# Kernel tuning notes

Hardware: AMD Instinct MI355X
Metric: run time of the kernel (lower is better)

Reference implementation:

```python
import jax, jax.numpy as jnp
import numpy as np

NUM_MODELS = 64
IN_F, HID, OUT_F = 6, 64, 3
LAYERS = 5
LN_EPS = 1e-5


def _mm_linear(x, W, B, idx):
    # W: [M, out, in], B: [M, out], x: [N, in], idx: [N]
    return jnp.einsum('nof,nf->no', W[idx], x) + B[idx]


def _mm_layernorm(x, g, b, idx):
    mu = jnp.mean(x, axis=-1, keepdims=True)
    var = jnp.mean((x - mu) ** 2, axis=-1, keepdims=True)
    xn = (x - mu) * jax.lax.rsqrt(var + LN_EPS)
    return xn * g[idx] + b[idx]


def setup_inputs() -> dict:
    key = jax.random.key(0)
    ks = jax.random.split(key, 16)
    N = 262144
    sqrt_k = float(np.sqrt(1.0 / NUM_MODELS))
    u = lambda k, shape: jax.random.uniform(k, shape, jnp.float32, -sqrt_k, sqrt_k)
    inp = {
        'x': jax.random.normal(ks[0], (N, IN_F), jnp.float32),
        'indices': jax.random.randint(ks[1], (N,), 0, NUM_MODELS),
        'W0': u(ks[2], (NUM_MODELS, HID, IN_F)), 'B0': u(ks[3], (NUM_MODELS, HID)),
        'G0': jnp.ones((NUM_MODELS, HID), jnp.float32), 'H0': jnp.zeros((NUM_MODELS, HID), jnp.float32),
        'W1': u(ks[4], (NUM_MODELS, HID, HID)), 'B1': u(ks[5], (NUM_MODELS, HID)),
        'G1': jnp.ones((NUM_MODELS, HID), jnp.float32), 'H1': jnp.zeros((NUM_MODELS, HID), jnp.float32),
        'W2': u(ks[6], (NUM_MODELS, HID, HID)), 'B2': u(ks[7], (NUM_MODELS, HID)),
        'G2': jnp.ones((NUM_MODELS, HID), jnp.float32), 'H2': jnp.zeros((NUM_MODELS, HID), jnp.float32),
        'W3': u(ks[8], (NUM_MODELS, HID, HID)), 'B3': u(ks[9], (NUM_MODELS, HID)),
        'G3': jnp.ones((NUM_MODELS, HID), jnp.float32), 'H3': jnp.zeros((NUM_MODELS, HID), jnp.float32),
        'W4': u(ks[10], (NUM_MODELS, OUT_F, HID)), 'B4': u(ks[11], (NUM_MODELS, OUT_F)),
    }
    return inp


def reference(x, indices, W0, B0, G0, H0, W1, B1, G1, H1, W2, B2, G2, H2, W3, B3, G3, H3, W4, B4):
    # forward_through_layers with use_layernorm=True, layers=5:
    Ws = [(W0, B0, G0, H0), (W1, B1, G1, H1), (W2, B2, G2, H2), (W3, B3, G3, H3)]
    h = x
    for W, B, G, Hb in Ws:
        h = _mm_linear(h, W, B, indices)
        h = _mm_layernorm(h, G, Hb, indices)
        h = jax.nn.relu(h)
    return _mm_linear(h, W4, B4, indices)  # [N, 3]
```

## Files before the change

kernel.cpp:

```cpp
#include <hip/hip_runtime.h>


#define NM    64
#define HIDD  64
#define INF   6
#define OUTF  3
#define CAP   4864
#define NBLKB 128

#define CSTRIDE   32
#define O_CURSORS 0
#define O_ORDER   2048
#define IWS_INTS  (O_ORDER + NM * CAP)

#define CONST_B   30720
#define NCONSTF   784
#define IMG_BYTES 33856

typedef _Float16 v8h __attribute__((ext_vector_type(8)));
typedef __fp16   v2hf __attribute__((ext_vector_type(2)));
typedef float    v4f __attribute__((ext_vector_type(4)));

struct BF { v8h lo, hi; };
struct PK2 { v2hf a, b; };

__device__ __host__ __forceinline__ int phi(int p) {
    int mt = p >> 4, q = (p >> 2) & 3, r = p & 3;
    return ((mt >> 1) << 5) | (q << 3) | ((mt & 1) << 2) | r;
}

__global__ __launch_bounds__(256, 4) void bucket_img_kernel(
    const int* __restrict__ idx, const float* __restrict__ x, int n,
    const float* __restrict__ W0, const float* __restrict__ W1,
    const float* __restrict__ W2, const float* __restrict__ W3,
    const float* __restrict__ W4,
    const float* __restrict__ B0, const float* __restrict__ G0, const float* __restrict__ H0,
    const float* __restrict__ B1, const float* __restrict__ G1, const float* __restrict__ H1,
    const float* __restrict__ B2, const float* __restrict__ G2, const float* __restrict__ H2,
    const float* __restrict__ B3, const float* __restrict__ G3, const float* __restrict__ H3,
    const float* __restrict__ B4,
    int* __restrict__ iws, _Float16* __restrict__ xs,
    unsigned char* __restrict__ imgbase) {
    __shared__ int lcnt[NM], lcur[NM];
    const int b = blockIdx.x, t = threadIdx.x;
    const int m = b >> 1, sub = b & 1;

    _Float16* img = (_Float16*)(imgbase + (size_t)m * IMG_BYTES);
    float* cst = (float*)(imgbase + (size_t)m * IMG_BYTES + CONST_B);
    for (int s = sub * 256 + t; s < 1920; s += 512) {
        int f = s >> 6, l = s & 63;
        int c = l & 15, q = l >> 4;
        float vals[8];
        if (f < 4) {
            const float* wr = W0 + m * 384 + phi(f * 16 + c) * 6;
#pragma unroll
            for (int j = 0; j < 8; j++) {
                int k = q * 8 + j;
                vals[j] = (k < INF) ? wr[k] : 0.0f;
            }
        } else if (f < 28) {
            int ll = (f - 4) >> 3, fb = (f - 4) & 7;
            int mt = fb >> 1, kh = fb & 1;
            const float* W = (ll == 0) ? W1 : (ll == 1) ? W2 : W3;
            const float* wr = W + m * 4096 + phi(mt * 16 + c) * 64 + kh * 32 + q * 8;
#pragma unroll
            for (int j = 0; j < 8; j++) vals[j] = wr[j];
        } else {
            int kh = f - 28;
            const float* wr = W4 + m * 192 + c * 64 + kh * 32 + q * 8;
#pragma unroll
            for (int j = 0; j < 8; j++) vals[j] = (c < OUTF) ? wr[j] : 0.0f;
        }
        v8h o;
#pragma unroll
        for (int j = 0; j < 8; j++) o[j] = (_Float16)vals[j];
        *(v8h*)(img + (size_t)s * 8) = o;
    }
    for (int e = sub * 256 + t; e < NCONSTF; e += 512) {
        const float* lsrc[12] = {B0, G0, H0, B1, G1, H1, B2, G2, H2, B3, G3, H3};
        float v = 0.0f;
        if (e < 768) {
            int l = e / 192, r = e - l * 192;
            v = lsrc[l * 3 + (r >> 6)][m * 64 + phi(r & 63)];
        } else if (e < 771) {
            v = B4[m * 3 + (e - 768)];
        }
        cst[e] = v;
    }

    if (t < NM) lcnt[t] = 0;
    __syncthreads();
    const int per = (n + NBLKB - 1) / NBLKB;
    const int beg = b * per, end = min(n, beg + per);
    for (int i = beg + t; i < end; i += 256) atomicAdd(&lcnt[idx[i]], 1);
    __syncthreads();
    if (t < NM) lcur[t] = atomicAdd(&iws[O_CURSORS + t * CSTRIDE], lcnt[t]);
    __syncthreads();
    for (int i = beg + t; i < end; i += 256) {
        int mm = idx[i];
        int r = atomicAdd(&lcur[mm], 1);
        int slot = mm * CAP + r;
        iws[O_ORDER + slot] = i;
        const float* xp = x + (size_t)i * 6;
        float2 a0 = *(const float2*)(xp);
        float2 a1 = *(const float2*)(xp + 2);
        float2 a2 = *(const float2*)(xp + 4);
        v8h o = {};
        o[0] = (_Float16)a0.x; o[1] = (_Float16)a0.y;
        o[2] = (_Float16)a1.x; o[3] = (_Float16)a1.y;
        o[4] = (_Float16)a2.x; o[5] = (_Float16)a2.y;
        *(v8h*)(xs + (size_t)slot * 8) = o;
    }
}

#define MFMA16(A, B, C) __builtin_amdgcn_mfma_f32_16x16x32_f16((A), (B), (C), 0, 0, 0)

__device__ __forceinline__ PK2 epi_quad(v4f dd, const float* gp, const float* hp,
                                        float rs, float nm) {
    v4f g = *(const v4f*)gp;
    v4f h = *(const v4f*)hp;
    float y0 = fmaxf(fmaf(fmaf(dd[0], rs, nm), g[0], h[0]), 0.0f);
    float y1 = fmaxf(fmaf(fmaf(dd[1], rs, nm), g[1], h[1]), 0.0f);
    float y2 = fmaxf(fmaf(fmaf(dd[2], rs, nm), g[2], h[2]), 0.0f);
    float y3 = fmaxf(fmaf(fmaf(dd[3], rs, nm), g[3], h[3]), 0.0f);
    PK2 r;
    r.a = __builtin_amdgcn_cvt_pkrtz(y0, y1);
    r.b = __builtin_amdgcn_cvt_pkrtz(y2, y3);
    return r;
}

__device__ __forceinline__ BF layer_epilogue(v4f d0, v4f d1, v4f d2, v4f d3,
                                             const float* cb, int q) {
    float S = 0.0f, Q2 = 0.0f;
#pragma unroll
    for (int r = 0; r < 4; r++) {
        S += d0[r]; S += d1[r]; S += d2[r]; S += d3[r];
        Q2 = fmaf(d0[r], d0[r], Q2);
        Q2 = fmaf(d1[r], d1[r], Q2);
        Q2 = fmaf(d2[r], d2[r], Q2);
        Q2 = fmaf(d3[r], d3[r], Q2);
    }
    S += __shfl_xor(S, 16, 64);
    S += __shfl_xor(S, 32, 64);
    Q2 += __shfl_xor(Q2, 16, 64);
    Q2 += __shfl_xor(Q2, 32, 64);
    float mu = S * (1.0f / 64.0f);
    float var = Q2 * (1.0f / 64.0f) - mu * mu;
    float rs = rsqrtf(var + 1e-5f);
    float nm = -mu * rs;
    PK2 p0 = epi_quad(d0, cb + 64 + 0  + q * 4, cb + 128 + 0  + q * 4, rs, nm);
    PK2 p1 = epi_quad(d1, cb + 64 + 16 + q * 4, cb + 128 + 16 + q * 4, rs, nm);
    PK2 p2 = epi_quad(d2, cb + 64 + 32 + q * 4, cb + 128 + 32 + q * 4, rs, nm);
    PK2 p3 = epi_quad(d3, cb + 64 + 48 + q * 4, cb + 128 + 48 + q * 4, rs, nm);
    BF o;
    o.lo[0] = p0.a[0]; o.lo[1] = p0.a[1]; o.lo[2] = p0.b[0]; o.lo[3] = p0.b[1];
    o.lo[4] = p1.a[0]; o.lo[5] = p1.a[1]; o.lo[6] = p1.b[0]; o.lo[7] = p1.b[1];
    o.hi[0] = p2.a[0]; o.hi[1] = p2.a[1]; o.hi[2] = p2.b[0]; o.hi[3] = p2.b[1];
    o.hi[4] = p3.a[0]; o.hi[5] = p3.a[1]; o.hi[6] = p3.b[0]; o.hi[7] = p3.b[1];
    return o;
}

__device__ __forceinline__ BF l0_sample(const _Float16* xs, int sp, int q,
                                        v8h A0, v8h A1, v8h A2, v8h A3,
                                        v4f b0, v4f b1, v4f b2, v4f b3,
                                        const float* cf) {
    v8h bfr = {};
    if (q == 0) bfr = *(const v8h*)(xs + (size_t)sp * 8);
    v4f d0 = MFMA16(A0, bfr, b0);
    v4f d1 = MFMA16(A1, bfr, b1);
    v4f d2 = MFMA16(A2, bfr, b2);
    v4f d3 = MFMA16(A3, bfr, b3);
    return layer_epilogue(d0, d1, d2, d3, cf, q);
}

__device__ __forceinline__ BF mid_sample(BF h,
                                         v8h a00, v8h a01, v8h a10, v8h a11,
                                         v8h a20, v8h a21, v8h a30, v8h a31,
                                         v4f b0, v4f b1, v4f b2, v4f b3,
                                         const float* cb, int q) {
    v4f d0 = MFMA16(a00, h.lo, b0); d0 = MFMA16(a01, h.hi, d0);
    v4f d1 = MFMA16(a10, h.lo, b1); d1 = MFMA16(a11, h.hi, d1);
    v4f d2 = MFMA16(a20, h.lo, b2); d2 = MFMA16(a21, h.hi, d2);
    v4f d3 = MFMA16(a30, h.lo, b3); d3 = MFMA16(a31, h.hi, d3);
    return layer_epilogue(d0, d1, d2, d3, cb, q);
}

__global__ __launch_bounds__(256, 3) void mlp_kernel(
    const int* __restrict__ iws, const _Float16* __restrict__ xs,
    const unsigned char* __restrict__ imgbase, float* __restrict__ out) {
    const int m = blockIdx.y;
    const int cnt = iws[O_CURSORS + m * CSTRIDE];
    const int beg = m * CAP, end = beg + cnt;
    const int base = beg + blockIdx.x * 256;
    if (base >= end) return;

    const int t = threadIdx.x, w = t >> 6, lane = t & 63;
    const int c = lane & 15, q = lane >> 4;
    const int wbase = base + w * 64;
    if (wbase >= end) return;

    const _Float16* img = (const _Float16*)(imgbase + (size_t)m * IMG_BYTES);
    const float* cf = (const float*)(imgbase + (size_t)m * IMG_BYTES + CONST_B);
    const int* order = iws + O_ORDER;

    const int p0i = wbase + 0 + c,  p1i = wbase + 16 + c;
    const int p2i = wbase + 32 + c, p3i = wbase + 48 + c;
    const int sp0 = p0i < end ? p0i : end - 1;
    const int sp1 = p1i < end ? p1i : end - 1;
    const int sp2 = p2i < end ? p2i : end - 1;
    const int sp3 = p3i < end ? p3i : end - 1;
    const int sid0 = order[sp0], sid1 = order[sp1];
    const int sid2 = order[sp2], sid3 = order[sp3];

    BF h0, h1, h2, h3;

    {
        v8h A0 = *(const v8h*)(img + 0 * 512 + lane * 8);
        v8h A1 = *(const v8h*)(img + 1 * 512 + lane * 8);
        v8h A2 = *(const v8h*)(img + 2 * 512 + lane * 8);
        v8h A3 = *(const v8h*)(img + 3 * 512 + lane * 8);
        v4f b0 = *(const v4f*)(cf + 0  + q * 4);
        v4f b1 = *(const v4f*)(cf + 16 + q * 4);
        v4f b2 = *(const v4f*)(cf + 32 + q * 4);
        v4f b3 = *(const v4f*)(cf + 48 + q * 4);
        h0 = l0_sample(xs, sp0, q, A0, A1, A2, A3, b0, b1, b2, b3, cf);
        h1 = l0_sample(xs, sp1, q, A0, A1, A2, A3, b0, b1, b2, b3, cf);
        h2 = l0_sample(xs, sp2, q, A0, A1, A2, A3, b0, b1, b2, b3, cf);
        h3 = l0_sample(xs, sp3, q, A0, A1, A2, A3, b0, b1, b2, b3, cf);
    }

    for (int l = 1; l <= 3; l++) {
        const _Float16* wp = img + 2048 + (l - 1) * 4096 + lane * 8;
        v8h a00 = *(const v8h*)(wp + 0 * 512);
        v8h a01 = *(const v8h*)(wp + 1 * 512);
        v8h a10 = *(const v8h*)(wp + 2 * 512);
        v8h a11 = *(const v8h*)(wp + 3 * 512);
        v8h a20 = *(const v8h*)(wp + 4 * 512);
        v8h a21 = *(const v8h*)(wp + 5 * 512);
        v8h a30 = *(const v8h*)(wp + 6 * 512);
        v8h a31 = *(const v8h*)(wp + 7 * 512);
        const float* cb = cf + l * 192;
        v4f b0 = *(const v4f*)(cb + 0  + q * 4);
        v4f b1 = *(const v4f*)(cb + 16 + q * 4);
        v4f b2 = *(const v4f*)(cb + 32 + q * 4);
        v4f b3 = *(const v4f*)(cb + 48 + q * 4);
        h0 = mid_sample(h0, a00, a01, a10, a11, a20, a21, a30, a31, b0, b1, b2, b3, cb, q);
        h1 = mid_sample(h1, a00, a01, a10, a11, a20, a21, a30, a31, b0, b1, b2, b3, cb, q);
        h2 = mid_sample(h2, a00, a01, a10, a11, a20, a21, a30, a31, b0, b1, b2, b3, cb, q);
        h3 = mid_sample(h3, a00, a01, a10, a11, a20, a21, a30, a31, b0, b1, b2, b3, cb, q);
    }

    {
        const _Float16* wp = img + 14336 + lane * 8;
        v8h A0 = *(const v8h*)(wp);
        v8h A1 = *(const v8h*)(wp + 512);
        v4f b4i = {cf[768], cf[769], cf[770], 0.0f};
        v4f D0 = MFMA16(A0, h0.lo, b4i); D0 = MFMA16(A1, h0.hi, D0);
        v4f D1 = MFMA16(A0, h1.lo, b4i); D1 = MFMA16(A1, h1.hi, D1);
        v4f D2 = MFMA16(A0, h2.lo, b4i); D2 = MFMA16(A1, h2.hi, D2);
        v4f D3 = MFMA16(A0, h3.lo, b4i); D3 = MFMA16(A1, h3.hi, D3);
        if (q == 0) {
            if (p0i < end) { float* op = out + (size_t)sid0 * 3; op[0] = D0[0]; op[1] = D0[1]; op[2] = D0[2]; }
            if (p1i < end) { float* op = out + (size_t)sid1 * 3; op[0] = D1[0]; op[1] = D1[1]; op[2] = D1[2]; }
            if (p2i < end) { float* op = out + (size_t)sid2 * 3; op[0] = D2[0]; op[1] = D2[1]; op[2] = D2[2]; }
            if (p3i < end) { float* op = out + (size_t)sid3 * 3; op[0] = D3[0]; op[1] = D3[1]; op[2] = D3[2]; }
        }
    }
}

extern "C" void kernel_launch(void* const* d_in, const int* in_sizes, int n_in,
                              void* d_out, int out_size, void* d_ws, size_t ws_size,
                              hipStream_t stream) {
    const float* x  = (const float*)d_in[0];
    const int*  idx = (const int*)d_in[1];
    const float* W0 = (const float*)d_in[2];
    const float* B0 = (const float*)d_in[3];
    const float* G0 = (const float*)d_in[4];
    const float* H0 = (const float*)d_in[5];
    const float* W1 = (const float*)d_in[6];
    const float* B1 = (const float*)d_in[7];
    const float* G1 = (const float*)d_in[8];
    const float* H1 = (const float*)d_in[9];
    const float* W2 = (const float*)d_in[10];
    const float* B2 = (const float*)d_in[11];
    const float* G2 = (const float*)d_in[12];
    const float* H2 = (const float*)d_in[13];
    const float* W3 = (const float*)d_in[14];
    const float* B3 = (const float*)d_in[15];
    const float* G3 = (const float*)d_in[16];
    const float* H3 = (const float*)d_in[17];
    const float* W4 = (const float*)d_in[18];
    const float* B4 = (const float*)d_in[19];
    float* out = (float*)d_out;

    int n = in_sizes[1];
    int* iws = (int*)d_ws;
    _Float16* xs = (_Float16*)((char*)d_ws + (size_t)IWS_INTS * 4);
    unsigned char* imgbase =
        (unsigned char*)d_ws + (size_t)IWS_INTS * 4 + (size_t)NM * CAP * 16;

    (void)hipMemsetAsync(d_ws, 0, NM * CSTRIDE * sizeof(int), stream);
    bucket_img_kernel<<<dim3(NBLKB), 256, 0, stream>>>(
        idx, x, n, W0, W1, W2, W3, W4,
        B0, G0, H0, B1, G1, H1, B2, G2, H2, B3, G3, H3, B4, iws, xs, imgbase);
    mlp_kernel<<<dim3(19, NM), 256, 0, stream>>>(iws, xs, imgbase, out);
}
```

Baseline: 131.7 us.

## Split per-model bucket cursors into four regions to cut global atomic contention

Each model's bucket now has four cursors, and the four block classes fill regions growing from both ends of the two halves of the bucket capacity. This spreads the global atomicAdd traffic over more addresses. The bucketing kernel also doubles its block count to 256, each block sized for a quarter of a model's image work. The MLP kernel reconstructs validity from the four counts and skips empty tiles, and the middle-layer loop is unrolled. The risks are a gap region in the middle of each bucket that wastes some tile work, and more complex validity checks.

```diff
diff --git a/kernel.cpp b/kernel.cpp
--- a/kernel.cpp
+++ b/kernel.cpp
@@ -6,11 +6,12 @@
 #define INF   6
 #define OUTF  3
 #define CAP   4864
-#define NBLKB 128
+#define RHALF 2432
+#define NBLKB 256
 
 #define CSTRIDE   32
 #define O_CURSORS 0
-#define O_ORDER   2048
+#define O_ORDER   8192
 #define IWS_INTS  (O_ORDER + NM * CAP)
 
 #define CONST_B   30720
@@ -43,11 +44,12 @@
     unsigned char* __restrict__ imgbase) {
     __shared__ int lcnt[NM], lcur[NM];
     const int b = blockIdx.x, t = threadIdx.x;
-    const int m = b >> 1, sub = b & 1;
+    const int m = b >> 2, sub = b & 3;
+    const int cls = b & 3;
 
     _Float16* img = (_Float16*)(imgbase + (size_t)m * IMG_BYTES);
     float* cst = (float*)(imgbase + (size_t)m * IMG_BYTES + CONST_B);
-    for (int s = sub * 256 + t; s < 1920; s += 512) {
+    for (int s = sub * 256 + t; s < 1920; s += 1024) {
         int f = s >> 6, l = s & 63;
         int c = l & 15, q = l >> 4;
         float vals[8];
@@ -76,30 +78,40 @@
         for (int j = 0; j < 8; j++) o[j] = (_Float16)vals[j];
         *(v8h*)(img + (size_t)s * 8) = o;
     }
-    for (int e = sub * 256 + t; e < NCONSTF; e += 512) {
+    {
         const float* lsrc[12] = {B0, G0, H0, B1, G1, H1, B2, G2, H2, B3, G3, H3};
-        float v = 0.0f;
-        if (e < 768) {
-            int l = e / 192, r = e - l * 192;
-            v = lsrc[l * 3 + (r >> 6)][m * 64 + phi(r & 63)];
-        } else if (e < 771) {
-            v = B4[m * 3 + (e - 768)];
+        int e = sub * 256 + t;
+        if (e < NCONSTF) {
+            float v = 0.0f;
+            if (e < 768) {
+                int l = e / 192, r = e - l * 192;
+                v = lsrc[l * 3 + (r >> 6)][m * 64 + phi(r & 63)];
+            } else if (e < 771) {
+                v = B4[m * 3 + (e - 768)];
+            }
+            cst[e] = v;
         }
-        cst[e] = v;
-    }
-
-    if (t < NM) lcnt[t] = 0;
+    }
+
+    if (t < NM) { lcnt[t] = 0; lcur[t] = 0; }
     __syncthreads();
     const int per = (n + NBLKB - 1) / NBLKB;
     const int beg = b * per, end = min(n, beg + per);
     for (int i = beg + t; i < end; i += 256) atomicAdd(&lcnt[idx[i]], 1);
     __syncthreads();
-    if (t < NM) lcur[t] = atomicAdd(&iws[O_CURSORS + t * CSTRIDE], lcnt[t]);
+    __shared__ int lbase[NM];
+    if (t < NM)
+        lbase[t] = atomicAdd(&iws[O_CURSORS + (t * 4 + cls) * CSTRIDE], lcnt[t]);
     __syncthreads();
     for (int i = beg + t; i < end; i += 256) {
         int mm = idx[i];
         int r = atomicAdd(&lcur[mm], 1);
-        int slot = mm * CAP + r;
+        int rel;
+        if (cls == 0)      rel = lbase[mm] + r;
+        else if (cls == 1) rel = RHALF - lbase[mm] - lcnt[mm] + r;
+        else if (cls == 2) rel = RHALF + lbase[mm] + r;
+        else               rel = CAP - lbase[mm] - lcnt[mm] + r;
+        int slot = mm * CAP + rel;
         iws[O_ORDER + slot] = i;
         const float* xp = x + (size_t)i * 6;
         float2 a0 = *(const float2*)(xp);
@@ -160,12 +172,12 @@
     return o;
 }
 
-__device__ __forceinline__ BF l0_sample(const _Float16* xs, int sp, int q,
+__device__ __forceinline__ BF l0_sample(const _Float16* xs, int slot, int q,
                                         v8h A0, v8h A1, v8h A2, v8h A3,
                                         v4f b0, v4f b1, v4f b2, v4f b3,
                                         const float* cf) {
     v8h bfr = {};
-    if (q == 0) bfr = *(const v8h*)(xs + (size_t)sp * 8);
+    if (q == 0) bfr = *(const v8h*)(xs + (size_t)slot * 8);
     v4f d0 = MFMA16(A0, bfr, b0);
     v4f d1 = MFMA16(A1, bfr, b1);
     v4f d2 = MFMA16(A2, bfr, b2);
@@ -185,32 +197,44 @@
     return layer_epilogue(d0, d1, d2, d3, cb, q);
 }
 
+__device__ __forceinline__ int in_valid(int rel, int a0, int a1, int a2, int a3) {
+    return (rel < a0) | ((rel >= RHALF - a1) & (rel < RHALF + a2)) |
+           (rel >= CAP - a3);
+}
+
 __global__ __launch_bounds__(256, 3) void mlp_kernel(
     const int* __restrict__ iws, const _Float16* __restrict__ xs,
     const unsigned char* __restrict__ imgbase, float* __restrict__ out) {
     const int m = blockIdx.y;
-    const int cnt = iws[O_CURSORS + m * CSTRIDE];
-    const int beg = m * CAP, end = beg + cnt;
-    const int base = beg + blockIdx.x * 256;
-    if (base >= end) return;
+    const int a0 = iws[O_CURSORS + (m * 4 + 0) * CSTRIDE];
+    const int a1 = iws[O_CURSORS + (m * 4 + 1) * CSTRIDE];
+    const int a2 = iws[O_CURSORS + (m * 4 + 2) * CSTRIDE];
+    const int a3 = iws[O_CURSORS + (m * 4 + 3) * CSTRIDE];
+    const int C0 = blockIdx.x * 256, C1 = C0 + 256;
+    if (!((C0 < a0) | ((C1 > RHALF - a1) & (C0 < RHALF + a2)) | (C1 > CAP - a3)))
+        return;
 
     const int t = threadIdx.x, w = t >> 6, lane = t & 63;
     const int c = lane & 15, q = lane >> 4;
-    const int wbase = base + w * 64;
-    if (wbase >= end) return;
+    const int wb = C0 + w * 64;
+    if (!((wb < a0) | ((wb + 64 > RHALF - a1) & (wb < RHALF + a2)) |
+          (wb + 64 > CAP - a3)))
+        return;
 
     const _Float16* img = (const _Float16*)(imgbase + (size_t)m * IMG_BYTES);
     const float* cf = (const float*)(imgbase + (size_t)m * IMG_BYTES + CONST_B);
     const int* order = iws + O_ORDER;
 
-    const int p0i = wbase + 0 + c,  p1i = wbase + 16 + c;
-    const int p2i = wbase + 32 + c, p3i = wbase + 48 + c;
-    const int sp0 = p0i < end ? p0i : end - 1;
-    const int sp1 = p1i < end ? p1i : end - 1;
-    const int sp2 = p2i < end ? p2i : end - 1;
-    const int sp3 = p3i < end ? p3i : end - 1;
-    const int sid0 = order[sp0], sid1 = order[sp1];
-    const int sid2 = order[sp2], sid3 = order[sp3];
+    const int r0 = wb + 0 + c,  r1 = wb + 16 + c;
+    const int r2 = wb + 32 + c, r3 = wb + 48 + c;
+    const int v0 = in_valid(r0, a0, a1, a2, a3);
+    const int v1 = in_valid(r1, a0, a1, a2, a3);
+    const int v2 = in_valid(r2, a0, a1, a2, a3);
+    const int v3 = in_valid(r3, a0, a1, a2, a3);
+    const int s0 = m * CAP + r0, s1 = m * CAP + r1;
+    const int s2 = m * CAP + r2, s3 = m * CAP + r3;
+    const int sid0 = order[s0], sid1 = order[s1];
+    const int sid2 = order[s2], sid3 = order[s3];
 
     BF h0, h1, h2, h3;
 
@@ -223,12 +247,13 @@
         v4f b1 = *(const v4f*)(cf + 16 + q * 4);
         v4f b2 = *(const v4f*)(cf + 32 + q * 4);
         v4f b3 = *(const v4f*)(cf + 48 + q * 4);
-        h0 = l0_sample(xs, sp0, q, A0, A1, A2, A3, b0, b1, b2, b3, cf);
-        h1 = l0_sample(xs, sp1, q, A0, A1, A2, A3, b0, b1, b2, b3, cf);
-        h2 = l0_sample(xs, sp2, q, A0, A1, A2, A3, b0, b1, b2, b3, cf);
-        h3 = l0_sample(xs, sp3, q, A0, A1, A2, A3, b0, b1, b2, b3, cf);
-    }
-
+        h0 = l0_sample(xs, s0, q, A0, A1, A2, A3, b0, b1, b2, b3, cf);
+        h1 = l0_sample(xs, s1, q, A0, A1, A2, A3, b0, b1, b2, b3, cf);
+        h2 = l0_sample(xs, s2, q, A0, A1, A2, A3, b0, b1, b2, b3, cf);
+        h3 = l0_sample(xs, s3, q, A0, A1, A2, A3, b0, b1, b2, b3, cf);
+    }
+
+#pragma unroll
     for (int l = 1; l <= 3; l++) {
         const _Float16* wp = img + 2048 + (l - 1) * 4096 + lane * 8;
         v8h a00 = *(const v8h*)(wp + 0 * 512);
@@ -260,10 +285,10 @@
         v4f D2 = MFMA16(A0, h2.lo, b4i); D2 = MFMA16(A1, h2.hi, D2);
         v4f D3 = MFMA16(A0, h3.lo, b4i); D3 = MFMA16(A1, h3.hi, D3);
         if (q == 0) {
-            if (p0i < end) { float* op = out + (size_t)sid0 * 3; op[0] = D0[0]; op[1] = D0[1]; op[2] = D0[2]; }
-            if (p1i < end) { float* op = out + (size_t)sid1 * 3; op[0] = D1[0]; op[1] = D1[1]; op[2] = D1[2]; }
-            if (p2i < end) { float* op = out + (size_t)sid2 * 3; op[0] = D2[0]; op[1] = D2[1]; op[2] = D2[2]; }
-            if (p3i < end) { float* op = out + (size_t)sid3 * 3; op[0] = D3[0]; op[1] = D3[1]; op[2] = D3[2]; }
+            if (v0) { float* op = out + (size_t)sid0 * 3; op[0] = D0[0]; op[1] = D0[1]; op[2] = D0[2]; }
+            if (v1) { float* op = out + (size_t)sid1 * 3; op[0] = D1[0]; op[1] = D1[1]; op[2] = D1[2]; }
+            if (v2) { float* op = out + (size_t)sid2 * 3; op[0] = D2[0]; op[1] = D2[1]; op[2] = D2[2]; }
+            if (v3) { float* op = out + (size_t)sid3 * 3; op[0] = D3[0]; op[1] = D3[1]; op[2] = D3[2]; }
         }
     }
 }
@@ -299,7 +324,7 @@
     unsigned char* imgbase =
         (unsigned char*)d_ws + (size_t)IWS_INTS * 4 + (size_t)NM * CAP * 16;
 
-    (void)hipMemsetAsync(d_ws, 0, NM * CSTRIDE * sizeof(int), stream);
+    (void)hipMemsetAsync(d_ws, 0, NM * 4 * CSTRIDE * sizeof(int), stream);
     bucket_img_kernel<<<dim3(NBLKB), 256, 0, stream>>>(
         idx, x, n, W0, W1, W2, W3, W4,
         B0, G0, H0, B1, G1, H1, B2, G2, H2, B3, G3, H3, B4, iws, xs, imgbase);
```

Result: faster. 127.8 us (-2.9%).
